# Optimization experiments

Measured on AMD Instinct MI355X. Metric: run time of the kernel, lower is better.

## Reference

```python
import jax, jax.numpy as jnp
import numpy as np

G = 256        # graphs per batch
N = 256        # nodes per graph (max_n for dense padding)
D = 256        # node_hidden_dim
H = 8          # num_heads
EPS = 1e-5


def _layer_norm(h, g, b):
    mu = jnp.mean(h, axis=-1, keepdims=True)
    var = jnp.mean((h - mu) ** 2, axis=-1, keepdims=True)
    return (h - mu) * jax.lax.rsqrt(var + EPS) * g + b


def setup_inputs() -> dict:
    key = jax.random.key(0)
    ks = jax.random.split(key, 16)
    s = 0.02
    inp = {
        "x": jax.random.normal(ks[0], (G * N, D), dtype=jnp.float32),
        "batch": jnp.repeat(jnp.arange(G, dtype=jnp.int32), N),  # sorted segment ids
        "batch_CLS": jax.random.normal(ks[1], (G, 1, D), dtype=jnp.float32),
        "Wq": jax.random.normal(ks[2], (D, D), dtype=jnp.float32) * s,
        "bq": jnp.zeros((D,), jnp.float32),
        "Wk": jax.random.normal(ks[3], (D, D), dtype=jnp.float32) * s,
        "bk": jnp.zeros((D,), jnp.float32),
        "Wv": jax.random.normal(ks[4], (D, D), dtype=jnp.float32) * s,
        "bv": jnp.zeros((D,), jnp.float32),
        "Wo": jax.random.normal(ks[5], (D, D), dtype=jnp.float32) * s,
        "bo": jnp.zeros((D,), jnp.float32),
        "g0": jnp.ones((D,), jnp.float32),
        "beta0": jnp.zeros((D,), jnp.float32),
        "W1": jax.random.normal(ks[6], (D, 2 * D), dtype=jnp.float32) * s,
        "b1": jnp.zeros((2 * D,), jnp.float32),
        "W2": jax.random.normal(ks[7], (2 * D, D), dtype=jnp.float32) * s,
        "b2": jnp.zeros((D,), jnp.float32),
        "g1": jnp.ones((D,), jnp.float32),
        "beta1": jnp.zeros((D,), jnp.float32),
    }
    return inp


def reference(x, batch, batch_CLS, Wq, bq, Wk, bk, Wv, bv, Wo, bo,
              g0, beta0, W1, b1, W2, b2, g1, beta1):
    total = x.shape[0]
    batch = batch.astype(jnp.int32)

    # ---- to_dense_batch: scatter nodes into [G, N, D] padded tensor + mask
    counts = jax.ops.segment_sum(jnp.ones((total,), jnp.int32), batch, num_segments=G)
    start = jnp.concatenate([jnp.zeros((1,), jnp.int32), jnp.cumsum(counts)[:-1]])
    pos = jnp.arange(total, dtype=jnp.int32) - start[batch]  # position within graph
    x_dense = jnp.zeros((G, N, D), x.dtype).at[batch, pos].set(x)
    mask = jnp.zeros((G, N), bool).at[batch, pos].set(True)

    # ---- append CLS token per graph
    x_dense = jnp.concatenate([x_dense, batch_CLS], axis=1)            # [G, N+1, D]
    attn_mask = jnp.concatenate([mask, jnp.ones((G, 1), bool)], axis=1)  # [G, N+1]

    # ---- masked multi-head self-attention (split/cat pattern == head reshape)
    dh = D // H
    Q = (x_dense @ Wq + bq).reshape(G, N + 1, H, dh)
    K = (x_dense @ Wk + bk).reshape(G, N + 1, H, dh)
    V = (x_dense @ Wv + bv).reshape(G, N + 1, H, dh)
    scores = jnp.einsum('bqhd,bkhd->bhqk', Q, K) / np.sqrt(dh).astype(np.float32)
    inf_mask = jnp.where(attn_mask, 0.0, -1e9)[:, None, None, :]        # [G,1,1,N+1]
    A = jax.nn.softmax(scores + inf_mask, axis=-1)
    attn = jnp.einsum('bhqk,bkhd->bqhd', A, V).reshape(G, N + 1, D)
    attn = attn @ Wo + bo

    # ---- residual, split CLS back off, gather dense->sparse
    attn = attn + x_dense
    cls = attn[:, -1, :]                       # [G, D]
    nodes = attn[:, :-1, :][batch, pos]        # [total, D] (inverse of to_dense_batch)
    h = jnp.concatenate([nodes, cls], axis=0)  # [total + G, D]

    h = _layer_norm(h, g0, beta0)
    f = jax.nn.relu(h @ W1 + b1) @ W2 + b2
    out = _layer_norm(f + h, g1, beta1)
    return out
```

## Files before the change

### kernel.cpp

```cpp
#include <hip/hip_runtime.h>

typedef __attribute__((ext_vector_type(8))) short short8;
typedef __attribute__((ext_vector_type(8))) unsigned short ushort8;
typedef __attribute__((ext_vector_type(4))) float f32x4;
typedef unsigned short ushort;
typedef unsigned int uint;

#define QSCALE 0.17677669529663687f

__device__ __forceinline__ ushort f2bf(float f) {
  union { float f; unsigned u; } a; a.f = f;
  unsigned r = a.u + 0x7fffu + ((a.u >> 16) & 1u);
  return (ushort)(r >> 16);
}
__device__ __forceinline__ float bf2f(ushort u) {
  union { uint u; float f; } a; a.u = ((uint)u) << 16; return a.f;
}
__device__ __forceinline__ uint cvtpk(float a, float b) {
  uint r; asm("v_cvt_pk_bf16_f32 %0, %1, %2" : "=v"(r) : "v"(a), "v"(b)); return r;
}

__device__ __forceinline__ void gload16(const void* g, void* l) {
  __builtin_amdgcn_global_load_lds((const __attribute__((address_space(1))) void*)g,
                                   (__attribute__((address_space(3))) void*)l, 16, 0, 0);
}

__device__ __forceinline__ uint xcd_swz(uint hwid, uint nwg) {
  const uint q8 = nwg >> 3, r8 = nwg & 7;
  const uint xcd = hwid & 7, i8 = hwid >> 3;
  return (xcd < r8 ? xcd * (q8 + 1) : r8 * (q8 + 1) + (xcd - r8) * q8) + i8;
}

__global__ __launch_bounds__(256) void seg_start_k(const int* __restrict__ batch,
                                                   int* __restrict__ start) {
  const int i = blockIdx.x * 256 + threadIdx.x;
  const int b = batch[i];
  if (i == 0 || batch[i - 1] != b) start[b] = i;
  if (i == 0) start[256] = 65536;
}

__global__ __launch_bounds__(256) void prep_w_k(
    const float* __restrict__ Wq, const float* __restrict__ Wk,
    const float* __restrict__ Wv, const float* __restrict__ Wo,
    const float* __restrict__ W1, const float* __restrict__ W2,
    ushort* __restrict__ Wt) {
  const int w = blockIdx.y;
  const float* src; ushort* dst; int Kd, Nd; float sc = 1.0f;
  switch (w) {
    case 0: src = Wq; dst = Wt;          Kd = 256; Nd = 256; sc = QSCALE; break;
    case 1: src = Wk; dst = Wt + 65536;  Kd = 256; Nd = 256; break;
    case 2: src = Wv; dst = Wt + 131072; Kd = 256; Nd = 256; break;
    case 3: src = Wo; dst = Wt + 196608; Kd = 256; Nd = 256; break;
    case 4: src = W1; dst = Wt + 262144; Kd = 256; Nd = 512; break;
    default: src = W2; dst = Wt + 393216; Kd = 512; Nd = 256; break;
  }
  const int e = blockIdx.x * 256 + threadIdx.x;
  if (e < Kd * Nd) {
    const int k = e / Nd, n = e - k * Nd;
    dst[n * Kd + k] = f2bf(src[e] * sc);
  }
}

__global__ __launch_bounds__(256) void pack_xd_k(
    const float* __restrict__ x, const float* __restrict__ cls,
    const int* __restrict__ start, ushort* __restrict__ xd) {
  const size_t idx = (((size_t)blockIdx.x << 8) + threadIdx.x) << 3;
  const int row = (int)(idx >> 8);
  const int col = (int)(idx & 255);
  const int g = row / 257, n = row - g * 257;
  const int sg = start[g], cn = start[g + 1] - sg;
  float4 a, b;
  if (n < cn) {
    const float* src = x + (((size_t)(sg + n)) << 8) + col;
    a = ((const float4*)src)[0]; b = ((const float4*)src)[1];
  } else if (n == 256) {
    const float* src = cls + (((size_t)g) << 8) + col;
    a = ((const float4*)src)[0]; b = ((const float4*)src)[1];
  } else {
    a.x = a.y = a.z = a.w = 0.f; b = a;
  }
  ushort8 o;
  o[0] = f2bf(a.x); o[1] = f2bf(a.y); o[2] = f2bf(a.z); o[3] = f2bf(a.w);
  o[4] = f2bf(b.x); o[5] = f2bf(b.y); o[6] = f2bf(b.z); o[7] = f2bf(b.w);
  *(ushort8*)(xd + idx) = o;
}

template<int EPI>
__device__ __forceinline__ void gemm_body(
    const ushort* __restrict__ A, const ushort* __restrict__ Bt,
    int N, int K,
    const float* __restrict__ b0, const float* __restrict__ b1, const float* __restrict__ b2,
    ushort* __restrict__ o0, ushort* __restrict__ o1, ushort* __restrict__ o2,
    float* __restrict__ of32,
    const float* __restrict__ x, const float* __restrict__ cls,
    const int* __restrict__ start, const ushort* __restrict__ resid,
    const float* __restrict__ gamma, const float* __restrict__ beta) {
  __shared__ __align__(16) char As[2][16384];
  __shared__ __align__(16) char Bs[2][32768];
  const int tid = threadIdx.x, lane = tid & 63, wid = tid >> 6;
  const int hi = lane >> 4, lc = lane & 15;
  const int wm = wid >> 2, wn = wid & 3;

  const uint nx = gridDim.x, ny = gridDim.y;
  const uint hwid = blockIdx.y * nx + blockIdx.x;
  const uint wg = xcd_swz(hwid, nx * ny);
  const int bx = wg / ny, by = wg % ny;

  const int m0 = bx * 128;
  const int n0 = (EPI == 0) ? 0 : by * 256;
  const int z = (EPI == 0) ? by : 0;
  const ushort* Bz = (EPI == 0) ? Bt + (size_t)z * 65536 : Bt;
  const float* bias = (EPI == 0) ? (z == 0 ? b0 : (z == 1 ? b1 : b2)) : b0;
  const float bmul = (EPI == 0 && z == 0) ? QSCALE : 1.0f;
  ushort* obf = (EPI == 0) ? (z == 0 ? o0 : (z == 1 ? o1 : o2)) : o0;

  f32x4 acc[4][4];
#pragma unroll
  for (int a = 0; a < 4; ++a)
#pragma unroll
    for (int b = 0; b < 4; ++b) acc[a][b] = (f32x4)0.0f;

  auto STAGE = [&](int bs, int kt) {
#pragma unroll
    for (int r = 0; r < 2; ++r) {
      const int L = r * 8192 + tid * 16;
      const int row = L >> 7;
      const int cb = (L & 127) ^ ((row & 7) << 4);
      gload16(A + (size_t)(m0 + row) * K + kt + (cb >> 1), As[bs] + L);
    }
#pragma unroll
    for (int r = 0; r < 4; ++r) {
      const int L = r * 8192 + tid * 16;
      const int row = L >> 7;
      const int cb = (L & 127) ^ ((row & 7) << 4);
      gload16(Bz + (size_t)(n0 + row) * K + kt + (cb >> 1), Bs[bs] + L);
    }
  };
  auto COMPUTE = [&](int bs) {
#pragma unroll
    for (int ks = 0; ks < 2; ++ks) {
      short8 af[4], bfr[4];
      const int cB = (ks * 32 + hi * 8) * 2;
#pragma unroll
      for (int t = 0; t < 4; ++t) {
        const int rA = wm * 64 + t * 16 + lc;
        af[t] = *(const short8*)(As[bs] + (rA << 7) + (cB ^ ((rA & 7) << 4)));
        const int rB = wn * 64 + t * 16 + lc;
        bfr[t] = *(const short8*)(Bs[bs] + (rB << 7) + (cB ^ ((rB & 7) << 4)));
      }
#pragma unroll
      for (int mt = 0; mt < 4; ++mt)
#pragma unroll
        for (int nt = 0; nt < 4; ++nt)
          acc[mt][nt] = __builtin_amdgcn_mfma_f32_16x16x32_bf16(af[mt], bfr[nt], acc[mt][nt], 0, 0, 0);
    }
  };

  STAGE(0, 0);
  asm volatile("s_waitcnt vmcnt(0)" ::: "memory");
  __syncthreads();
  int cur = 0;
  for (int kt = 64; kt < K; kt += 64) {
    STAGE(cur ^ 1, kt);
    COMPUTE(cur);
    asm volatile("s_waitcnt vmcnt(0)" ::: "memory");
    __syncthreads();
    cur ^= 1;
  }
  COMPUTE(cur);

  if constexpr (EPI == 0 || EPI == 2) {
#pragma unroll
    for (int mt = 0; mt < 4; ++mt)
#pragma unroll
      for (int i = 0; i < 4; ++i) {
        const int m = m0 + wm * 64 + mt * 16 + hi * 4 + i;
#pragma unroll
        for (int nt = 0; nt < 4; ++nt) {
          const int n = (EPI == 0 ? 0 : n0) + wn * 64 + nt * 16 + lc;
          const float v = acc[mt][nt][i] + bias[n] * bmul;
          obf[(size_t)m * N + n] = f2bf(EPI == 2 ? fmaxf(v, 0.0f) : v);
        }
      }
  } else {
#pragma unroll
    for (int mt = 0; mt < 4; ++mt)
#pragma unroll
      for (int i = 0; i < 4; ++i) {
        const int m = m0 + wm * 64 + mt * 16 + hi * 4 + i;
        int gg = 0, nr = 0, sg = 0, cn = 0;
        if constexpr (EPI == 1) {
          gg = m / 257; nr = m - gg * 257; sg = start[gg]; cn = start[gg + 1] - sg;
        }
#pragma unroll
        for (int nt = 0; nt < 4; ++nt) {
          const int n = wn * 64 + nt * 16 + lc;
          float res;
          if constexpr (EPI == 1)
            res = (nr < cn) ? x[((size_t)(sg + nr) << 8) + n]
                            : (nr == 256 ? cls[((size_t)gg << 8) + n] : 0.0f);
          else
            res = bf2f(resid[((size_t)m << 8) + n]);
          acc[mt][nt][i] += bias[n] + res;
        }
      }
    __syncthreads();
    float* red = (float*)As;
#pragma unroll
    for (int mt = 0; mt < 4; ++mt)
#pragma unroll
      for (int i = 0; i < 4; ++i) {
        float s = 0.f, ss = 0.f;
#pragma unroll
        for (int nt = 0; nt < 4; ++nt) {
          const float v = acc[mt][nt][i];
          s += v; ss += v * v;
        }
#pragma unroll
        for (int mk = 1; mk < 16; mk <<= 1) {
          s += __shfl_xor(s, mk); ss += __shfl_xor(ss, mk);
        }
        if (lc == 0) {
          const int idx = ((wm * 64 + mt * 16 + hi * 4 + i) * 4 + wn) * 2;
          red[idx] = s; red[idx + 1] = ss;
        }
      }
    __syncthreads();
#pragma unroll
    for (int mt = 0; mt < 4; ++mt)
#pragma unroll
      for (int i = 0; i < 4; ++i) {
        const int r64 = mt * 16 + hi * 4 + i;
        const int m = m0 + wm * 64 + r64;
        const float* rp = red + ((wm * 64 + r64) * 4) * 2;
        const float sum = rp[0] + rp[2] + rp[4] + rp[6];
        const float ssq = rp[1] + rp[3] + rp[5] + rp[7];
        const float mu = sum * (1.0f / 256.0f);
        const float rs = rsqrtf(ssq * (1.0f / 256.0f) - mu * mu + 1e-5f);
        size_t r2 = (size_t)m;
        bool wr = true;
        if constexpr (EPI == 1) {
          const int gg = m / 257, nr = m - gg * 257;
          const int sg = start[gg], cn = start[gg + 1] - sg;
          if (nr < cn) r2 = (size_t)(sg + nr);
          else if (nr == 256) r2 = (size_t)(65536 + gg);
          else wr = false;
        }
#pragma unroll
        for (int nt = 0; nt < 4; ++nt) {
          const int n = wn * 64 + nt * 16 + lc;
          const float o = (acc[mt][nt][i] - mu) * rs * gamma[n] + beta[n];
          if constexpr (EPI == 1) {
            if (wr) o0[(r2 << 8) + n] = f2bf(o);
          } else {
            of32[((size_t)m << 8) + n] = o;
          }
        }
      }
  }
}

__global__ __launch_bounds__(512) void gemm_qkv(
    const ushort* A, const ushort* Bt, const float* bq, const float* bk, const float* bv,
    ushort* Q, ushort* K, ushort* V) {
  gemm_body<0>(A, Bt, 256, 256, bq, bk, bv, Q, K, V,
               nullptr, nullptr, nullptr, nullptr, nullptr, nullptr, nullptr);
}
__global__ __launch_bounds__(512) void gemm_wo_ln(
    const ushort* A, const ushort* Bt, const float* bo,
    ushort* h16, const float* x, const float* cls, const int* start,
    const float* gamma, const float* beta) {
  gemm_body<1>(A, Bt, 256, 256, bo, nullptr, nullptr, h16, nullptr, nullptr,
               nullptr, x, cls, start, nullptr, gamma, beta);
}
__global__ __launch_bounds__(512) void gemm_ffn1(
    const ushort* A, const ushort* Bt, const float* b1, ushort* t16) {
  gemm_body<2>(A, Bt, 512, 256, b1, nullptr, nullptr, t16, nullptr, nullptr,
               nullptr, nullptr, nullptr, nullptr, nullptr, nullptr, nullptr);
}
__global__ __launch_bounds__(512) void gemm_ffn2_ln(
    const ushort* A, const ushort* Bt, const float* b2,
    float* out, const ushort* resid, const float* gamma, const float* beta) {
  gemm_body<3>(A, Bt, 256, 512, b2, nullptr, nullptr, nullptr, nullptr, nullptr,
               out, nullptr, nullptr, nullptr, resid, gamma, beta);
}

#define KSTR 40
#define VSTR 296
#define OSTR 40
__global__ __launch_bounds__(512) void attn_k(
    const ushort* __restrict__ Q, const ushort* Kb,
    const ushort* __restrict__ Vb, const int* __restrict__ start,
    ushort* O) {
  __shared__ __align__(16) ushort Ks[272 * KSTR];
  __shared__ __align__(16) ushort Vt[32 * VSTR];
  __shared__ __align__(16) ushort Ot[8][16 * OSTR];
  const int tid = threadIdx.x, lane = tid & 63, wid = tid >> 6;
  const int hi = lane >> 4, lo = lane & 15;
  const uint wg = xcd_swz(blockIdx.x, 2048);
  const int g = wg >> 3, h = wg & 7;
  const int cnt = start[g + 1] - start[g];
  const size_t base = ((size_t)g * 257) * 256 + h * 32;

  for (int n = tid; n < 272; n += 512) {
    const bool rv = (n < cnt) || (n == 256);
    if (n < 257 && rv) {
      const ushort* src = Kb + base + ((size_t)n << 8);
#pragma unroll
      for (int j = 0; j < 4; ++j)
        *(ushort8*)(Ks + n * KSTR + j * 8) = *(const ushort8*)(src + j * 8);
    } else {
      const ushort8 zz = (ushort8)0;
#pragma unroll
      for (int j = 0; j < 4; ++j) *(ushort8*)(Ks + n * KSTR + j * 8) = zz;
    }
  }
  for (int it = tid; it < 1152; it += 512) {
    const int n = it >> 2, d0 = (it & 3) * 8;
    const bool rv = (n < cnt) || (n == 256);
    ushort8 v8;
    if (n < 257 && rv) v8 = *(const ushort8*)(Vb + base + ((size_t)n << 8) + d0);
    else v8 = (ushort8)0;
#pragma unroll
    for (int j = 0; j < 8; ++j) Vt[(d0 + j) * VSTR + n] = v8[j];
  }
  __syncthreads();

  for (int qt = wid; qt < 17; qt += 8) {
    const int qr = qt * 16 + lo;
    const int qc = qr < 257 ? qr : 256;
    const short8 qf = *(const short8*)(Q + base + ((size_t)qc << 8) + hi * 8);

    float den = -(float)(271 - cnt);
    uint ds_[17][2];
#pragma unroll
    for (int kt = 0; kt < 17; ++kt) {
      const short8 kf = *(const short8*)(Ks + (kt * 16 + lo) * KSTR + hi * 8);
      const f32x4 st = __builtin_amdgcn_mfma_f32_16x16x32_bf16(kf, qf, (f32x4)0.0f, 0, 0, 0);
      const float e0 = __expf(st[0]), e1 = __expf(st[1]);
      const float e2 = __expf(st[2]), e3 = __expf(st[3]);
      den += (e0 + e1) + (e2 + e3);
      ds_[kt][0] = cvtpk(e0, e1);
      ds_[kt][1] = cvtpk(e2, e3);
    }
    den += __shfl_xor(den, 16);
    den += __shfl_xor(den, 32);
    const float inv = 1.0f / den;

    f32x4 ot0 = (f32x4)0.0f, ot1 = (f32x4)0.0f;
#pragma unroll
    for (int ks = 0; ks < 9; ++ks) {
      union { uint u[4]; short8 s8; } pb;
#pragma unroll
      for (int jp = 0; jp < 4; ++jp) {
        const int sl = lo | ((((hi & 1) << 1) | (jp >> 1)) << 4);
        if (ks < 8) {
          const uint a = (uint)__shfl((int)ds_[2 * ks][jp & 1], sl);
          const uint b = (uint)__shfl((int)ds_[2 * ks + 1][jp & 1], sl);
          pb.u[jp] = (hi < 2) ? a : b;
        } else {
          const uint a = (uint)__shfl((int)ds_[16][jp & 1], sl);
          pb.u[jp] = (hi < 2) ? a : 0u;
        }
      }
      const short8 va0 = *(const short8*)(Vt + lo * VSTR + ks * 32 + hi * 8);
      const short8 va1 = *(const short8*)(Vt + (16 + lo) * VSTR + ks * 32 + hi * 8);
      ot0 = __builtin_amdgcn_mfma_f32_16x16x32_bf16(va0, pb.s8, ot0, 0, 0, 0);
      ot1 = __builtin_amdgcn_mfma_f32_16x16x32_bf16(va1, pb.s8, ot1, 0, 0, 0);
    }

    {
      const uint w0 = cvtpk(ot0[0] * inv, ot0[1] * inv);
      const uint w1 = cvtpk(ot0[2] * inv, ot0[3] * inv);
      const uint w2 = cvtpk(ot1[0] * inv, ot1[1] * inv);
      const uint w3 = cvtpk(ot1[2] * inv, ot1[3] * inv);
      ushort* ob = Ot[wid] + lo * OSTR + hi * 4;
      *(uint*)(ob + 0) = w0;
      *(uint*)(ob + 2) = w1;
      *(uint*)(ob + 16) = w2;
      *(uint*)(ob + 18) = w3;
    }
    asm volatile("s_waitcnt lgkmcnt(0)" ::: "memory");
    __builtin_amdgcn_sched_barrier(0);
    {
      const int r = lane >> 2;
      const int q2 = qt * 16 + r;
      const ushort8 ov = *(const ushort8*)(Ot[wid] + r * OSTR + (lane & 3) * 8);
      if (q2 < 257)
        *(ushort8*)(O + base + ((size_t)q2 << 8) + (lane & 3) * 8) = ov;
    }
    __builtin_amdgcn_sched_barrier(0);
  }
}

extern "C" void kernel_launch(void* const* d_in, const int* in_sizes, int n_in,
                              void* d_out, int out_size, void* d_ws, size_t ws_size,
                              hipStream_t stream) {
  (void)in_sizes; (void)n_in; (void)out_size; (void)ws_size;
  const float* x     = (const float*)d_in[0];
  const int*   batch = (const int*)d_in[1];
  const float* cls   = (const float*)d_in[2];
  const float* Wq    = (const float*)d_in[3];
  const float* bq    = (const float*)d_in[4];
  const float* Wk    = (const float*)d_in[5];
  const float* bk    = (const float*)d_in[6];
  const float* Wv    = (const float*)d_in[7];
  const float* bv    = (const float*)d_in[8];
  const float* Wo    = (const float*)d_in[9];
  const float* bo    = (const float*)d_in[10];
  const float* g0    = (const float*)d_in[11];
  const float* beta0 = (const float*)d_in[12];
  const float* W1    = (const float*)d_in[13];
  const float* b1    = (const float*)d_in[14];
  const float* W2    = (const float*)d_in[15];
  const float* b2    = (const float*)d_in[16];
  const float* g1    = (const float*)d_in[17];
  const float* beta1 = (const float*)d_in[18];

  char* ws = (char*)d_ws;
  int*    start = (int*)ws;
  ushort* Wt    = (ushort*)(ws + 4096);
  char*   sbase = ws + 1052672;
  ushort* Qb    = (ushort*)(sbase);
  ushort* Kb2   = (ushort*)(sbase + 33685504);
  ushort* Vb2   = (ushort*)(sbase + 67371008);
  ushort* h16   = Vb2;
  ushort* tmid  = Qb;
  ushort* xd    = (ushort*)d_out;
  float*  out   = (float*)d_out;

  seg_start_k<<<256, 256, 0, stream>>>(batch, start);
  prep_w_k<<<dim3(512, 6), 256, 0, stream>>>(Wq, Wk, Wv, Wo, W1, W2, Wt);
  pack_xd_k<<<8224, 256, 0, stream>>>(x, cls, start, xd);
  gemm_qkv<<<dim3(514, 3), 512, 0, stream>>>(xd, Wt, bq, bk, bv, Qb, Kb2, Vb2);
  attn_k<<<2048, 512, 0, stream>>>(Qb, Kb2, Vb2, start, Kb2);
  gemm_wo_ln<<<dim3(514, 1), 512, 0, stream>>>(Kb2, Wt + 196608, bo,
      h16, x, cls, start, g0, beta0);
  gemm_ffn1<<<dim3(514, 2), 512, 0, stream>>>(h16, Wt + 262144, b1, tmid);
  gemm_ffn2_ln<<<dim3(514, 1), 512, 0, stream>>>(tmid, Wt + 393216, b2,
      out, h16, g1, beta1);
}
```

Before: 280.6 us.

## Split GEMMs into smaller single-buffered tiles with 256-thread blocks

Splits the shared GEMM body into two kernels. Plain-epilogue GEMMs (QKV, FFN1) now use 128x128 tiles with 4 waves, and the LayerNorm-epilogue GEMMs (Wo, FFN2) use 64x256 row tiles with 4 waves. Both drop the double-buffered LDS pipeline for a single buffer with load-wait-compute per K step. The aim is to cut LDS use and block size so more blocks fit per CU and the grid fills the GPU better, at the cost of losing overlap between global loads and MFMA work.

```diff
diff --git a/kernel.cpp b/kernel.cpp
--- a/kernel.cpp
+++ b/kernel.cpp
@@ -86,20 +86,16 @@
 }
 
 template<int EPI>
-__device__ __forceinline__ void gemm_body(
+__device__ __forceinline__ void gemm_a_body(
     const ushort* __restrict__ A, const ushort* __restrict__ Bt,
     int N, int K,
     const float* __restrict__ b0, const float* __restrict__ b1, const float* __restrict__ b2,
-    ushort* __restrict__ o0, ushort* __restrict__ o1, ushort* __restrict__ o2,
-    float* __restrict__ of32,
-    const float* __restrict__ x, const float* __restrict__ cls,
-    const int* __restrict__ start, const ushort* __restrict__ resid,
-    const float* __restrict__ gamma, const float* __restrict__ beta) {
-  __shared__ __align__(16) char As[2][16384];
-  __shared__ __align__(16) char Bs[2][32768];
+    ushort* __restrict__ o0, ushort* __restrict__ o1, ushort* __restrict__ o2) {
+  __shared__ __align__(16) char As[16384];
+  __shared__ __align__(16) char Bs[16384];
   const int tid = threadIdx.x, lane = tid & 63, wid = tid >> 6;
   const int hi = lane >> 4, lc = lane & 15;
-  const int wm = wid >> 2, wn = wid & 3;
+  const int wm = wid >> 1, wn = wid & 1;
 
   const uint nx = gridDim.x, ny = gridDim.y;
   const uint hwid = blockIdx.y * nx + blockIdx.x;
@@ -107,8 +103,8 @@
   const int bx = wg / ny, by = wg % ny;
 
   const int m0 = bx * 128;
-  const int n0 = (EPI == 0) ? 0 : by * 256;
-  const int z = (EPI == 0) ? by : 0;
+  const int z = (EPI == 0) ? (by >> 1) : 0;
+  const int ncol0 = (EPI == 0) ? (by & 1) * 128 : by * 128;
   const ushort* Bz = (EPI == 0) ? Bt + (size_t)z * 65536 : Bt;
   const float* bias = (EPI == 0) ? (z == 0 ? b0 : (z == 1 ? b1 : b2)) : b0;
   const float bmul = (EPI == 0 && z == 0) ? QSCALE : 1.0f;
@@ -120,23 +116,23 @@
 #pragma unroll
     for (int b = 0; b < 4; ++b) acc[a][b] = (f32x4)0.0f;
 
-  auto STAGE = [&](int bs, int kt) {
-#pragma unroll
-    for (int r = 0; r < 2; ++r) {
-      const int L = r * 8192 + tid * 16;
+  for (int kt = 0; kt < K; kt += 64) {
+#pragma unroll
+    for (int r = 0; r < 4; ++r) {
+      const int L = (r * 256 + tid) * 16;
       const int row = L >> 7;
       const int cb = (L & 127) ^ ((row & 7) << 4);
-      gload16(A + (size_t)(m0 + row) * K + kt + (cb >> 1), As[bs] + L);
+      gload16(A + (size_t)(m0 + row) * K + kt + (cb >> 1), As + L);
     }
 #pragma unroll
     for (int r = 0; r < 4; ++r) {
-      const int L = r * 8192 + tid * 16;
+      const int L = (r * 256 + tid) * 16;
       const int row = L >> 7;
       const int cb = (L & 127) ^ ((row & 7) << 4);
-      gload16(Bz + (size_t)(n0 + row) * K + kt + (cb >> 1), Bs[bs] + L);
-    }
-  };
-  auto COMPUTE = [&](int bs) {
+      gload16(Bz + (size_t)(ncol0 + row) * K + kt + (cb >> 1), Bs + L);
+    }
+    asm volatile("s_waitcnt vmcnt(0)" ::: "memory");
+    __syncthreads();
 #pragma unroll
     for (int ks = 0; ks < 2; ++ks) {
       short8 af[4], bfr[4];
@@ -144,9 +140,9 @@
 #pragma unroll
       for (int t = 0; t < 4; ++t) {
         const int rA = wm * 64 + t * 16 + lc;
-        af[t] = *(const short8*)(As[bs] + (rA << 7) + (cB ^ ((rA & 7) << 4)));
+        af[t] = *(const short8*)(As + (rA << 7) + (cB ^ ((rA & 7) << 4)));
         const int rB = wn * 64 + t * 16 + lc;
-        bfr[t] = *(const short8*)(Bs[bs] + (rB << 7) + (cB ^ ((rB & 7) << 4)));
+        bfr[t] = *(const short8*)(Bs + (rB << 7) + (cB ^ ((rB & 7) << 4)));
       }
 #pragma unroll
       for (int mt = 0; mt < 4; ++mt)
@@ -154,135 +150,178 @@
         for (int nt = 0; nt < 4; ++nt)
           acc[mt][nt] = __builtin_amdgcn_mfma_f32_16x16x32_bf16(af[mt], bfr[nt], acc[mt][nt], 0, 0, 0);
     }
-  };
-
-  STAGE(0, 0);
-  asm volatile("s_waitcnt vmcnt(0)" ::: "memory");
-  __syncthreads();
-  int cur = 0;
-  for (int kt = 64; kt < K; kt += 64) {
-    STAGE(cur ^ 1, kt);
-    COMPUTE(cur);
+    __syncthreads();
+  }
+
+#pragma unroll
+  for (int mt = 0; mt < 4; ++mt)
+#pragma unroll
+    for (int i = 0; i < 4; ++i) {
+      const int m = m0 + wm * 64 + mt * 16 + hi * 4 + i;
+#pragma unroll
+      for (int nt = 0; nt < 4; ++nt) {
+        const int n = ncol0 + wn * 64 + nt * 16 + lc;
+        const float v = acc[mt][nt][i] + bias[n] * bmul;
+        obf[(size_t)m * N + n] = f2bf(EPI == 2 ? fmaxf(v, 0.0f) : v);
+      }
+    }
+}
+
+__global__ __launch_bounds__(256) void gemm_qkv(
+    const ushort* A, const ushort* Bt, const float* bq, const float* bk, const float* bv,
+    ushort* Q, ushort* K, ushort* V) {
+  gemm_a_body<0>(A, Bt, 256, 256, bq, bk, bv, Q, K, V);
+}
+__global__ __launch_bounds__(256) void gemm_ffn1(
+    const ushort* A, const ushort* Bt, const float* b1, ushort* t16) {
+  gemm_a_body<2>(A, Bt, 512, 256, b1, nullptr, nullptr, t16, nullptr, nullptr);
+}
+
+template<int EPI>
+__device__ __forceinline__ void gemm_b_body(
+    const ushort* __restrict__ A, const ushort* __restrict__ Bt, int K,
+    const float* __restrict__ bias,
+    ushort* __restrict__ o16, float* __restrict__ of32,
+    const float* __restrict__ x, const float* __restrict__ cls,
+    const int* __restrict__ start, const ushort* __restrict__ resid,
+    const float* __restrict__ gamma, const float* __restrict__ beta) {
+  __shared__ __align__(16) char As[8192];
+  __shared__ __align__(16) char Bs[32768];
+  const int tid = threadIdx.x, lane = tid & 63, wid = tid >> 6;
+  const int hi = lane >> 4, lc = lane & 15;
+  const int wn = wid;
+
+  const uint wg = xcd_swz(blockIdx.x, gridDim.x);
+  const int m0 = wg * 64;
+
+  f32x4 acc[4][4];
+#pragma unroll
+  for (int a = 0; a < 4; ++a)
+#pragma unroll
+    for (int b = 0; b < 4; ++b) acc[a][b] = (f32x4)0.0f;
+
+  for (int kt = 0; kt < K; kt += 64) {
+#pragma unroll
+    for (int r = 0; r < 2; ++r) {
+      const int L = (r * 256 + tid) * 16;
+      const int row = L >> 7;
+      const int cb = (L & 127) ^ ((row & 7) << 4);
+      gload16(A + (size_t)(m0 + row) * K + kt + (cb >> 1), As + L);
+    }
+#pragma unroll
+    for (int r = 0; r < 8; ++r) {
+      const int L = (r * 256 + tid) * 16;
+      const int row = L >> 7;
+      const int cb = (L & 127) ^ ((row & 7) << 4);
+      gload16(Bt + (size_t)row * K + kt + (cb >> 1), Bs + L);
+    }
     asm volatile("s_waitcnt vmcnt(0)" ::: "memory");
     __syncthreads();
-    cur ^= 1;
-  }
-  COMPUTE(cur);
-
-  if constexpr (EPI == 0 || EPI == 2) {
-#pragma unroll
-    for (int mt = 0; mt < 4; ++mt)
-#pragma unroll
-      for (int i = 0; i < 4; ++i) {
-        const int m = m0 + wm * 64 + mt * 16 + hi * 4 + i;
-#pragma unroll
-        for (int nt = 0; nt < 4; ++nt) {
-          const int n = (EPI == 0 ? 0 : n0) + wn * 64 + nt * 16 + lc;
-          const float v = acc[mt][nt][i] + bias[n] * bmul;
-          obf[(size_t)m * N + n] = f2bf(EPI == 2 ? fmaxf(v, 0.0f) : v);
+#pragma unroll
+    for (int ks = 0; ks < 2; ++ks) {
+      short8 af[4], bfr[4];
+      const int cB = (ks * 32 + hi * 8) * 2;
+#pragma unroll
+      for (int t = 0; t < 4; ++t) {
+        const int rA = t * 16 + lc;
+        af[t] = *(const short8*)(As + (rA << 7) + (cB ^ ((rA & 7) << 4)));
+        const int rB = wn * 64 + t * 16 + lc;
+        bfr[t] = *(const short8*)(Bs + (rB << 7) + (cB ^ ((rB & 7) << 4)));
+      }
+#pragma unroll
+      for (int mt = 0; mt < 4; ++mt)
+#pragma unroll
+        for (int nt = 0; nt < 4; ++nt)
+          acc[mt][nt] = __builtin_amdgcn_mfma_f32_16x16x32_bf16(af[mt], bfr[nt], acc[mt][nt], 0, 0, 0);
+    }
+    __syncthreads();
+  }
+
+#pragma unroll
+  for (int mt = 0; mt < 4; ++mt)
+#pragma unroll
+    for (int i = 0; i < 4; ++i) {
+      const int m = m0 + mt * 16 + hi * 4 + i;
+      int gg = 0, nr = 0, sg = 0, cn = 0;
+      if constexpr (EPI == 1) {
+        gg = m / 257; nr = m - gg * 257; sg = start[gg]; cn = start[gg + 1] - sg;
+      }
+#pragma unroll
+      for (int nt = 0; nt < 4; ++nt) {
+        const int n = wn * 64 + nt * 16 + lc;
+        float res;
+        if constexpr (EPI == 1)
+          res = (nr < cn) ? x[((size_t)(sg + nr) << 8) + n]
+                          : (nr == 256 ? cls[((size_t)gg << 8) + n] : 0.0f);
+        else
+          res = bf2f(resid[((size_t)m << 8) + n]);
+        acc[mt][nt][i] += bias[n] + res;
+      }
+    }
+  float* red = (float*)As;
+#pragma unroll
+  for (int mt = 0; mt < 4; ++mt)
+#pragma unroll
+    for (int i = 0; i < 4; ++i) {
+      float s = 0.f, ss = 0.f;
+#pragma unroll
+      for (int nt = 0; nt < 4; ++nt) {
+        const float v = acc[mt][nt][i];
+        s += v; ss += v * v;
+      }
+#pragma unroll
+      for (int mk = 1; mk < 16; mk <<= 1) {
+        s += __shfl_xor(s, mk); ss += __shfl_xor(ss, mk);
+      }
+      if (lc == 0) {
+        const int idx = ((mt * 16 + hi * 4 + i) * 4 + wn) * 2;
+        red[idx] = s; red[idx + 1] = ss;
+      }
+    }
+  __syncthreads();
+#pragma unroll
+  for (int mt = 0; mt < 4; ++mt)
+#pragma unroll
+    for (int i = 0; i < 4; ++i) {
+      const int r64 = mt * 16 + hi * 4 + i;
+      const int m = m0 + r64;
+      const float* rp = red + (r64 * 4) * 2;
+      const float sum = rp[0] + rp[2] + rp[4] + rp[6];
+      const float ssq = rp[1] + rp[3] + rp[5] + rp[7];
+      const float mu = sum * (1.0f / 256.0f);
+      const float rs = rsqrtf(ssq * (1.0f / 256.0f) - mu * mu + 1e-5f);
+      size_t r2 = (size_t)m;
+      bool wr = true;
+      if constexpr (EPI == 1) {
+        const int gg = m / 257, nr = m - gg * 257;
+        const int sg = start[gg], cn = start[gg + 1] - sg;
+        if (nr < cn) r2 = (size_t)(sg + nr);
+        else if (nr == 256) r2 = (size_t)(65536 + gg);
+        else wr = false;
+      }
+#pragma unroll
+      for (int nt = 0; nt < 4; ++nt) {
+        const int n = wn * 64 + nt * 16 + lc;
+        const float o = (acc[mt][nt][i] - mu) * rs * gamma[n] + beta[n];
+        if constexpr (EPI == 1) {
+          if (wr) o16[(r2 << 8) + n] = f2bf(o);
+        } else {
+          of32[((size_t)m << 8) + n] = o;
         }
       }
-  } else {
-#pragma unroll
-    for (int mt = 0; mt < 4; ++mt)
-#pragma unroll
-      for (int i = 0; i < 4; ++i) {
-        const int m = m0 + wm * 64 + mt * 16 + hi * 4 + i;
-        int gg = 0, nr = 0, sg = 0, cn = 0;
-        if constexpr (EPI == 1) {
-          gg = m / 257; nr = m - gg * 257; sg = start[gg]; cn = start[gg + 1] - sg;
-        }
-#pragma unroll
-        for (int nt = 0; nt < 4; ++nt) {
-          const int n = wn * 64 + nt * 16 + lc;
-          float res;
-          if constexpr (EPI == 1)
-            res = (nr < cn) ? x[((size_t)(sg + nr) << 8) + n]
-                            : (nr == 256 ? cls[((size_t)gg << 8) + n] : 0.0f);
-          else
-            res = bf2f(resid[((size_t)m << 8) + n]);
-          acc[mt][nt][i] += bias[n] + res;
-        }
-      }
-    __syncthreads();
-    float* red = (float*)As;
-#pragma unroll
-    for (int mt = 0; mt < 4; ++mt)
-#pragma unroll
-      for (int i = 0; i < 4; ++i) {
-        float s = 0.f, ss = 0.f;
-#pragma unroll
-        for (int nt = 0; nt < 4; ++nt) {
-          const float v = acc[mt][nt][i];
-          s += v; ss += v * v;
-        }
-#pragma unroll
-        for (int mk = 1; mk < 16; mk <<= 1) {
-          s += __shfl_xor(s, mk); ss += __shfl_xor(ss, mk);
-        }
-        if (lc == 0) {
-          const int idx = ((wm * 64 + mt * 16 + hi * 4 + i) * 4 + wn) * 2;
-          red[idx] = s; red[idx + 1] = ss;
-        }
-      }
-    __syncthreads();
-#pragma unroll
-    for (int mt = 0; mt < 4; ++mt)
-#pragma unroll
-      for (int i = 0; i < 4; ++i) {
-        const int r64 = mt * 16 + hi * 4 + i;
-        const int m = m0 + wm * 64 + r64;
-        const float* rp = red + ((wm * 64 + r64) * 4) * 2;
-        const float sum = rp[0] + rp[2] + rp[4] + rp[6];
-        const float ssq = rp[1] + rp[3] + rp[5] + rp[7];
-        const float mu = sum * (1.0f / 256.0f);
-        const float rs = rsqrtf(ssq * (1.0f / 256.0f) - mu * mu + 1e-5f);
-        size_t r2 = (size_t)m;
-        bool wr = true;
-        if constexpr (EPI == 1) {
-          const int gg = m / 257, nr = m - gg * 257;
-          const int sg = start[gg], cn = start[gg + 1] - sg;
-          if (nr < cn) r2 = (size_t)(sg + nr);
-          else if (nr == 256) r2 = (size_t)(65536 + gg);
-          else wr = false;
-        }
-#pragma unroll
-        for (int nt = 0; nt < 4; ++nt) {
-          const int n = wn * 64 + nt * 16 + lc;
-          const float o = (acc[mt][nt][i] - mu) * rs * gamma[n] + beta[n];
-          if constexpr (EPI == 1) {
-            if (wr) o0[(r2 << 8) + n] = f2bf(o);
-          } else {
-            of32[((size_t)m << 8) + n] = o;
-          }
-        }
-      }
-  }
-}
-
-__global__ __launch_bounds__(512) void gemm_qkv(
-    const ushort* A, const ushort* Bt, const float* bq, const float* bk, const float* bv,
-    ushort* Q, ushort* K, ushort* V) {
-  gemm_body<0>(A, Bt, 256, 256, bq, bk, bv, Q, K, V,
-               nullptr, nullptr, nullptr, nullptr, nullptr, nullptr, nullptr);
-}
-__global__ __launch_bounds__(512) void gemm_wo_ln(
+    }
+}
+
+__global__ __launch_bounds__(256) void gemm_wo_ln(
     const ushort* A, const ushort* Bt, const float* bo,
     ushort* h16, const float* x, const float* cls, const int* start,
     const float* gamma, const float* beta) {
-  gemm_body<1>(A, Bt, 256, 256, bo, nullptr, nullptr, h16, nullptr, nullptr,
-               nullptr, x, cls, start, nullptr, gamma, beta);
-}
-__global__ __launch_bounds__(512) void gemm_ffn1(
-    const ushort* A, const ushort* Bt, const float* b1, ushort* t16) {
-  gemm_body<2>(A, Bt, 512, 256, b1, nullptr, nullptr, t16, nullptr, nullptr,
-               nullptr, nullptr, nullptr, nullptr, nullptr, nullptr, nullptr);
-}
-__global__ __launch_bounds__(512) void gemm_ffn2_ln(
+  gemm_b_body<1>(A, Bt, 256, bo, h16, nullptr, x, cls, start, nullptr, gamma, beta);
+}
+__global__ __launch_bounds__(256) void gemm_ffn2_ln(
     const ushort* A, const ushort* Bt, const float* b2,
     float* out, const ushort* resid, const float* gamma, const float* beta) {
-  gemm_body<3>(A, Bt, 256, 512, b2, nullptr, nullptr, nullptr, nullptr, nullptr,
-               out, nullptr, nullptr, nullptr, resid, gamma, beta);
+  gemm_b_body<3>(A, Bt, 512, b2, nullptr, out, nullptr, nullptr, nullptr, resid, gamma, beta);
 }
 
 #define KSTR 40
@@ -432,11 +471,11 @@
   seg_start_k<<<256, 256, 0, stream>>>(batch, start);
   prep_w_k<<<dim3(512, 6), 256, 0, stream>>>(Wq, Wk, Wv, Wo, W1, W2, Wt);
   pack_xd_k<<<8224, 256, 0, stream>>>(x, cls, start, xd);
-  gemm_qkv<<<dim3(514, 3), 512, 0, stream>>>(xd, Wt, bq, bk, bv, Qb, Kb2, Vb2);
+  gemm_qkv<<<dim3(514, 6), 256, 0, stream>>>(xd, Wt, bq, bk, bv, Qb, Kb2, Vb2);
   attn_k<<<2048, 512, 0, stream>>>(Qb, Kb2, Vb2, start, Kb2);
-  gemm_wo_ln<<<dim3(514, 1), 512, 0, stream>>>(Kb2, Wt + 196608, bo,
+  gemm_wo_ln<<<1028, 256, 0, stream>>>(Kb2, Wt + 196608, bo,
       h16, x, cls, start, g0, beta0);
-  gemm_ffn1<<<dim3(514, 2), 512, 0, stream>>>(h16, Wt + 262144, b1, tmid);
-  gemm_ffn2_ln<<<dim3(514, 1), 512, 0, stream>>>(tmid, Wt + 393216, b2,
+  gemm_ffn1<<<dim3(514, 4), 256, 0, stream>>>(h16, Wt + 262144, b1, tmid);
+  gemm_ffn2_ln<<<1028, 256, 0, stream>>>(tmid, Wt + 393216, b2,
       out, h16, g1, beta1);
 }
```

Result: faster. 266.8 us (-4.9%).

## Restructure GEMMs to 256-row tiles with global-direct A fragments and LDS-staged B

Applied to the files above, without the earlier changes.

The shared GEMM body is rewritten. Each block now has 1024 threads and covers 256 rows and all output columns, with the grid halved to match. Only the weight operand is staged in LDS, in 128-wide K chunks with an XOR swizzle; the activation fragments are read straight from global memory into registers, and the double-buffered A/B LDS pipeline is removed. The Wo+LayerNorm residual is now read from the packed bf16 dense input instead of gathering fp32 x/cls through segment offsets. This trades LDS traffic and smaller tiles for unpipelined global A loads, a sync after every chunk, and slightly lower residual precision.

```diff
diff --git a/kernel.cpp b/kernel.cpp
--- a/kernel.cpp
+++ b/kernel.cpp
@@ -86,17 +86,16 @@
 }
 
 template<int EPI>
-__device__ __forceinline__ void gemm_body(
+__device__ __forceinline__ void gemm_c_body(
     const ushort* __restrict__ A, const ushort* __restrict__ Bt,
     int N, int K,
     const float* __restrict__ b0, const float* __restrict__ b1, const float* __restrict__ b2,
     ushort* __restrict__ o0, ushort* __restrict__ o1, ushort* __restrict__ o2,
     float* __restrict__ of32,
-    const float* __restrict__ x, const float* __restrict__ cls,
-    const int* __restrict__ start, const ushort* __restrict__ resid,
+    const ushort* __restrict__ resid, const int* __restrict__ start,
     const float* __restrict__ gamma, const float* __restrict__ beta) {
-  __shared__ __align__(16) char As[2][16384];
-  __shared__ __align__(16) char Bs[2][32768];
+  __shared__ __align__(16) char Bb[65536];
+  __shared__ __align__(16) float red[2048];
   const int tid = threadIdx.x, lane = tid & 63, wid = tid >> 6;
   const int hi = lane >> 4, lc = lane & 15;
   const int wm = wid >> 2, wn = wid & 3;
@@ -104,11 +103,11 @@
   const uint nx = gridDim.x, ny = gridDim.y;
   const uint hwid = blockIdx.y * nx + blockIdx.x;
   const uint wg = xcd_swz(hwid, nx * ny);
-  const int bx = wg / ny, by = wg % ny;
-
-  const int m0 = bx * 128;
-  const int n0 = (EPI == 0) ? 0 : by * 256;
+  const int bx = (int)(wg % nx), by = (int)(wg / nx);
+
+  const int m0 = bx * 256;
   const int z = (EPI == 0) ? by : 0;
+  const int ncol0 = (EPI == 2) ? by * 256 : 0;
   const ushort* Bz = (EPI == 0) ? Bt + (size_t)z * 65536 : Bt;
   const float* bias = (EPI == 0) ? (z == 0 ? b0 : (z == 1 ? b1 : b2)) : b0;
   const float bmul = (EPI == 0 && z == 0) ? QSCALE : 1.0f;
@@ -120,33 +119,29 @@
 #pragma unroll
     for (int b = 0; b < 4; ++b) acc[a][b] = (f32x4)0.0f;
 
-  auto STAGE = [&](int bs, int kt) {
-#pragma unroll
-    for (int r = 0; r < 2; ++r) {
-      const int L = r * 8192 + tid * 16;
-      const int row = L >> 7;
-      const int cb = (L & 127) ^ ((row & 7) << 4);
-      gload16(A + (size_t)(m0 + row) * K + kt + (cb >> 1), As[bs] + L);
-    }
-#pragma unroll
-    for (int r = 0; r < 4; ++r) {
-      const int L = r * 8192 + tid * 16;
-      const int row = L >> 7;
-      const int cb = (L & 127) ^ ((row & 7) << 4);
-      gload16(Bz + (size_t)(n0 + row) * K + kt + (cb >> 1), Bs[bs] + L);
-    }
-  };
-  auto COMPUTE = [&](int bs) {
-#pragma unroll
-    for (int ks = 0; ks < 2; ++ks) {
+  const int KST = K >> 7;
+  for (int st = 0; st < KST; ++st) {
+#pragma unroll
+    for (int s = 0; s < 4; ++s) {
+      const int L = (s * 1024 + tid) * 16;
+      const int row = L >> 8;
+      const int off = L & 255;
+      const int kloc = (off ^ ((row & 7) << 4)) >> 1;
+      gload16(Bz + (size_t)(ncol0 + row) * K + st * 128 + kloc, Bb + L);
+    }
+    asm volatile("s_waitcnt vmcnt(0)" ::: "memory");
+    __syncthreads();
+#pragma unroll
+    for (int ksub = 0; ksub < 4; ++ksub) {
+      const int kg = st * 128 + ksub * 32 + hi * 8;
       short8 af[4], bfr[4];
-      const int cB = (ks * 32 + hi * 8) * 2;
+#pragma unroll
+      for (int t = 0; t < 4; ++t)
+        af[t] = *(const short8*)(A + (size_t)(m0 + wm * 64 + t * 16 + lc) * K + kg);
 #pragma unroll
       for (int t = 0; t < 4; ++t) {
-        const int rA = wm * 64 + t * 16 + lc;
-        af[t] = *(const short8*)(As[bs] + (rA << 7) + (cB ^ ((rA & 7) << 4)));
-        const int rB = wn * 64 + t * 16 + lc;
-        bfr[t] = *(const short8*)(Bs[bs] + (rB << 7) + (cB ^ ((rB & 7) << 4)));
+        const int n = wn * 64 + t * 16 + lc;
+        bfr[t] = *(const short8*)(Bb + n * 256 + (((ksub * 32 + hi * 8) * 2) ^ ((n & 7) << 4)));
       }
 #pragma unroll
       for (int mt = 0; mt < 4; ++mt)
@@ -154,20 +149,8 @@
         for (int nt = 0; nt < 4; ++nt)
           acc[mt][nt] = __builtin_amdgcn_mfma_f32_16x16x32_bf16(af[mt], bfr[nt], acc[mt][nt], 0, 0, 0);
     }
-  };
-
-  STAGE(0, 0);
-  asm volatile("s_waitcnt vmcnt(0)" ::: "memory");
-  __syncthreads();
-  int cur = 0;
-  for (int kt = 64; kt < K; kt += 64) {
-    STAGE(cur ^ 1, kt);
-    COMPUTE(cur);
-    asm volatile("s_waitcnt vmcnt(0)" ::: "memory");
-    __syncthreads();
-    cur ^= 1;
-  }
-  COMPUTE(cur);
+    if (st + 1 < KST) __syncthreads();
+  }
 
   if constexpr (EPI == 0 || EPI == 2) {
 #pragma unroll
@@ -177,7 +160,7 @@
         const int m = m0 + wm * 64 + mt * 16 + hi * 4 + i;
 #pragma unroll
         for (int nt = 0; nt < 4; ++nt) {
-          const int n = (EPI == 0 ? 0 : n0) + wn * 64 + nt * 16 + lc;
+          const int n = ncol0 + wn * 64 + nt * 16 + lc;
           const float v = acc[mt][nt][i] + bias[n] * bmul;
           obf[(size_t)m * N + n] = f2bf(EPI == 2 ? fmaxf(v, 0.0f) : v);
         }
@@ -188,24 +171,12 @@
 #pragma unroll
       for (int i = 0; i < 4; ++i) {
         const int m = m0 + wm * 64 + mt * 16 + hi * 4 + i;
-        int gg = 0, nr = 0, sg = 0, cn = 0;
-        if constexpr (EPI == 1) {
-          gg = m / 257; nr = m - gg * 257; sg = start[gg]; cn = start[gg + 1] - sg;
-        }
 #pragma unroll
         for (int nt = 0; nt < 4; ++nt) {
           const int n = wn * 64 + nt * 16 + lc;
-          float res;
-          if constexpr (EPI == 1)
-            res = (nr < cn) ? x[((size_t)(sg + nr) << 8) + n]
-                            : (nr == 256 ? cls[((size_t)gg << 8) + n] : 0.0f);
-          else
-            res = bf2f(resid[((size_t)m << 8) + n]);
-          acc[mt][nt][i] += bias[n] + res;
-        }
-      }
-    __syncthreads();
-    float* red = (float*)As;
+          acc[mt][nt][i] += bias[n] + bf2f(resid[((size_t)m << 8) + n]);
+        }
+      }
 #pragma unroll
     for (int mt = 0; mt < 4; ++mt)
 #pragma unroll
@@ -230,9 +201,9 @@
     for (int mt = 0; mt < 4; ++mt)
 #pragma unroll
       for (int i = 0; i < 4; ++i) {
-        const int r64 = mt * 16 + hi * 4 + i;
-        const int m = m0 + wm * 64 + r64;
-        const float* rp = red + ((wm * 64 + r64) * 4) * 2;
+        const int r256 = wm * 64 + mt * 16 + hi * 4 + i;
+        const int m = m0 + r256;
+        const float* rp = red + r256 * 8;
         const float sum = rp[0] + rp[2] + rp[4] + rp[6];
         const float ssq = rp[1] + rp[3] + rp[5] + rp[7];
         const float mu = sum * (1.0f / 256.0f);
@@ -260,29 +231,29 @@
   }
 }
 
-__global__ __launch_bounds__(512) void gemm_qkv(
+__global__ __launch_bounds__(1024) void gemm_qkv(
     const ushort* A, const ushort* Bt, const float* bq, const float* bk, const float* bv,
     ushort* Q, ushort* K, ushort* V) {
-  gemm_body<0>(A, Bt, 256, 256, bq, bk, bv, Q, K, V,
-               nullptr, nullptr, nullptr, nullptr, nullptr, nullptr, nullptr);
-}
-__global__ __launch_bounds__(512) void gemm_wo_ln(
+  gemm_c_body<0>(A, Bt, 256, 256, bq, bk, bv, Q, K, V,
+                 nullptr, nullptr, nullptr, nullptr, nullptr);
+}
+__global__ __launch_bounds__(1024) void gemm_wo_ln(
     const ushort* A, const ushort* Bt, const float* bo,
-    ushort* h16, const float* x, const float* cls, const int* start,
+    ushort* h16, const ushort* xd, const int* start,
     const float* gamma, const float* beta) {
-  gemm_body<1>(A, Bt, 256, 256, bo, nullptr, nullptr, h16, nullptr, nullptr,
-               nullptr, x, cls, start, nullptr, gamma, beta);
-}
-__global__ __launch_bounds__(512) void gemm_ffn1(
+  gemm_c_body<1>(A, Bt, 256, 256, bo, nullptr, nullptr, h16, nullptr, nullptr,
+                 nullptr, xd, start, gamma, beta);
+}
+__global__ __launch_bounds__(1024) void gemm_ffn1(
     const ushort* A, const ushort* Bt, const float* b1, ushort* t16) {
-  gemm_body<2>(A, Bt, 512, 256, b1, nullptr, nullptr, t16, nullptr, nullptr,
-               nullptr, nullptr, nullptr, nullptr, nullptr, nullptr, nullptr);
-}
-__global__ __launch_bounds__(512) void gemm_ffn2_ln(
+  gemm_c_body<2>(A, Bt, 512, 256, b1, nullptr, nullptr, t16, nullptr, nullptr,
+                 nullptr, nullptr, nullptr, nullptr, nullptr);
+}
+__global__ __launch_bounds__(1024) void gemm_ffn2_ln(
     const ushort* A, const ushort* Bt, const float* b2,
     float* out, const ushort* resid, const float* gamma, const float* beta) {
-  gemm_body<3>(A, Bt, 256, 512, b2, nullptr, nullptr, nullptr, nullptr, nullptr,
-               out, nullptr, nullptr, nullptr, resid, gamma, beta);
+  gemm_c_body<3>(A, Bt, 256, 512, b2, nullptr, nullptr, nullptr, nullptr, nullptr,
+                 out, resid, nullptr, gamma, beta);
 }
 
 #define KSTR 40
@@ -432,11 +403,11 @@
   seg_start_k<<<256, 256, 0, stream>>>(batch, start);
   prep_w_k<<<dim3(512, 6), 256, 0, stream>>>(Wq, Wk, Wv, Wo, W1, W2, Wt);
   pack_xd_k<<<8224, 256, 0, stream>>>(x, cls, start, xd);
-  gemm_qkv<<<dim3(514, 3), 512, 0, stream>>>(xd, Wt, bq, bk, bv, Qb, Kb2, Vb2);
+  gemm_qkv<<<dim3(257, 3), 1024, 0, stream>>>(xd, Wt, bq, bk, bv, Qb, Kb2, Vb2);
   attn_k<<<2048, 512, 0, stream>>>(Qb, Kb2, Vb2, start, Kb2);
-  gemm_wo_ln<<<dim3(514, 1), 512, 0, stream>>>(Kb2, Wt + 196608, bo,
-      h16, x, cls, start, g0, beta0);
-  gemm_ffn1<<<dim3(514, 2), 512, 0, stream>>>(h16, Wt + 262144, b1, tmid);
-  gemm_ffn2_ln<<<dim3(514, 1), 512, 0, stream>>>(tmid, Wt + 393216, b2,
+  gemm_wo_ln<<<257, 1024, 0, stream>>>(Kb2, Wt + 196608, bo,
+      h16, xd, start, g0, beta0);
+  gemm_ffn1<<<dim3(257, 2), 1024, 0, stream>>>(h16, Wt + 262144, b1, tmid);
+  gemm_ffn2_ln<<<257, 1024, 0, stream>>>(tmid, Wt + 393216, b2,
       out, h16, g1, beta1);
 }
```

Result: slower. 438.5 us (+56.2%).
